# Performance work log

Hardware: AMD Instinct MI355X
Metric: run time of the kernel (lower is better)

Reference implementation:

```python
import jax, jax.numpy as jnp
import numpy as np

N = 50000   # nodes
DEG = 16    # avg degree
E = N * DEG # edges
D = 64      # 2*vl, vl=32
EPS = 1e-12 # F.normalize eps


def setup_inputs() -> dict:
    key = jax.random.key(0)
    k1, k2, k3, k4 = jax.random.split(key, 4)
    ft_lv0 = jax.random.normal(k1, (N, D), dtype=jnp.float32)
    # fc weights: Linear(4*vl, 2*vl, bias=False) -> shape [2*vl, 4*vl] = [64, 128]
    W1 = jax.random.normal(k2, (D, 2 * D), dtype=jnp.float32) * 0.05
    W2 = jax.random.normal(k3, (D, 2 * D), dtype=jnp.float32) * 0.05
    # edge list: tgt[e] gathers ft[nbr[e]] and sums into node tgt[e]
    nbr = jax.random.randint(k4, (E,), 0, N, dtype=jnp.int32)
    tgt = jnp.repeat(jnp.arange(N, dtype=jnp.int32), DEG)  # sorted segment ids
    return {"ft_lv0": ft_lv0, "W1": W1, "W2": W2, "nbr": nbr, "tgt": tgt}


def _gcn_layer(ft, W, nbr, tgt, n_nodes):
    # sum-pool neighbor features: pool[n] = sum_{m in adj(n)} ft[m]
    pool = jax.ops.segment_sum(ft[nbr], tgt, num_segments=n_nodes)  # [N, D]
    # concat(node + pool, node * pool); pool==0 for isolated nodes reproduces
    # the original else-branch cat(node, zeros) exactly.
    z = jnp.concatenate([ft + pool, ft * pool], axis=-1)  # [N, 2D]
    return jax.nn.relu(z @ W.T)  # [N, D]


def reference(ft_lv0, W1, W2, nbr, tgt):
    n_nodes = ft_lv0.shape[0]
    ft_lv1 = _gcn_layer(ft_lv0, W1, nbr, tgt, n_nodes)
    ft_lv2 = _gcn_layer(ft_lv1, W2, nbr, tgt, n_nodes)
    # F.normalize(z, dim=-1): z / max(||z||_2, eps)
    norm = jnp.linalg.norm(ft_lv2, axis=-1, keepdims=True)
    return ft_lv2 / jnp.maximum(norm, EPS)
```

## Files before the change

kernel.cpp:

```cpp
#include <hip/hip_runtime.h>
#include <hip/hip_bf16.h>


#define N_NODES 50000
#define DEG 16
#define DIM 64
#define NTILES 3125

typedef __attribute__((ext_vector_type(8))) short short8;
typedef __attribute__((ext_vector_type(8))) unsigned short ushort8;
typedef __attribute__((ext_vector_type(4))) float f32x4;

__device__ __forceinline__ unsigned short f2b(float f) {
  unsigned int u = __float_as_uint(f);
  u = (u + 0x7FFFu + ((u >> 16) & 1u)) >> 16;
  return (unsigned short)u;
}
#define LOF(u) __uint_as_float((u) << 16)
#define HIF(u) __uint_as_float((u) & 0xFFFF0000u)

__global__ void cast_bf16(const float* __restrict__ in, unsigned short* __restrict__ out, int n4) {
  const int i = blockIdx.x * 256 + threadIdx.x;
  if (i < n4) {
    const float4 v = reinterpret_cast<const float4*>(in)[i];
    ushort4 o4;
    o4.x = f2b(v.x); o4.y = f2b(v.y); o4.z = f2b(v.z); o4.w = f2b(v.w);
    reinterpret_cast<ushort4*>(out)[i] = o4;
  }
}

__global__ void prep_w(const float* __restrict__ W1, const float* __restrict__ W2,
                       unsigned short* __restrict__ Wb) {
  const int task = blockIdx.x * 256 + threadIdx.x;
  if (task >= 2048) return;
  const int which = task >> 10;
  const int f = (task >> 6) & 15;
  const int l = task & 63;
  const int ct = f >> 2, ks = f & 3;
  const int wn = l & 15, wg = l >> 4;
  const float* W = which ? W2 : W1;
  const float* wp = W + (ct * 16 + wn) * 128 + ks * 32 + wg * 8;
  const float4 w0 = *(const float4*)wp;
  const float4 w1 = *(const float4*)(wp + 4);
  ushort8 o;
  o[0] = f2b(w0.x); o[1] = f2b(w0.y); o[2] = f2b(w0.z); o[3] = f2b(w0.w);
  o[4] = f2b(w1.x); o[5] = f2b(w1.y); o[6] = f2b(w1.z); o[7] = f2b(w1.w);
  *(ushort8*)(Wb + ((size_t)(which * 16 + f) * 64 + l) * 8) = o;
}

#define GATHER_AND_STAGE()                                                     \
  _Pragma("unroll 2")                                                          \
  for (int p = 0; p < 8; ++p) {                                                \
    const int rA = (base + 2 * p) * DEG;                                       \
    const int4 ia0 = *(const int4*)(nbr + rA);                                 \
    const int4 ia1 = *(const int4*)(nbr + rA + 4);                             \
    const int4 ia2 = *(const int4*)(nbr + rA + 8);                             \
    const int4 ia3 = *(const int4*)(nbr + rA + 12);                            \
    const int4 ib0 = *(const int4*)(nbr + rA + 16);                            \
    const int4 ib1 = *(const int4*)(nbr + rA + 20);                            \
    const int4 ib2 = *(const int4*)(nbr + rA + 24);                            \
    const int4 ib3 = *(const int4*)(nbr + rA + 28);                            \
    const unsigned int un  = ftp[(base + 2 * p + half) * 32 + c];              \
    const unsigned int v0  = ftp[(half ? ib0.x : ia0.x) * 32 + c];             \
    const unsigned int v1  = ftp[(half ? ib0.y : ia0.y) * 32 + c];             \
    const unsigned int v2  = ftp[(half ? ib0.z : ia0.z) * 32 + c];             \
    const unsigned int v3  = ftp[(half ? ib0.w : ia0.w) * 32 + c];             \
    const unsigned int v4  = ftp[(half ? ib1.x : ia1.x) * 32 + c];             \
    const unsigned int v5  = ftp[(half ? ib1.y : ia1.y) * 32 + c];             \
    const unsigned int v6  = ftp[(half ? ib1.z : ia1.z) * 32 + c];             \
    const unsigned int v7  = ftp[(half ? ib1.w : ia1.w) * 32 + c];             \
    const unsigned int v8  = ftp[(half ? ib2.x : ia2.x) * 32 + c];             \
    const unsigned int v9  = ftp[(half ? ib2.y : ia2.y) * 32 + c];             \
    const unsigned int v10 = ftp[(half ? ib2.z : ia2.z) * 32 + c];             \
    const unsigned int v11 = ftp[(half ? ib2.w : ia2.w) * 32 + c];             \
    const unsigned int v12 = ftp[(half ? ib3.x : ia3.x) * 32 + c];             \
    const unsigned int v13 = ftp[(half ? ib3.y : ia3.y) * 32 + c];             \
    const unsigned int v14 = ftp[(half ? ib3.z : ia3.z) * 32 + c];             \
    const unsigned int v15 = ftp[(half ? ib3.w : ia3.w) * 32 + c];             \
    const float plo = (((LOF(v0) + LOF(v1)) + (LOF(v2) + LOF(v3))) +           \
                       ((LOF(v4) + LOF(v5)) + (LOF(v6) + LOF(v7)))) +          \
                      (((LOF(v8) + LOF(v9)) + (LOF(v10) + LOF(v11))) +         \
                       ((LOF(v12) + LOF(v13)) + (LOF(v14) + LOF(v15))));       \
    const float phi = (((HIF(v0) + HIF(v1)) + (HIF(v2) + HIF(v3))) +           \
                       ((HIF(v4) + HIF(v5)) + (HIF(v6) + HIF(v7)))) +          \
                      (((HIF(v8) + HIF(v9)) + (HIF(v10) + HIF(v11))) +         \
                       ((HIF(v12) + HIF(v13)) + (HIF(v14) + HIF(v15))));       \
    const float nlo = LOF(un), nhi = HIF(un);                                  \
    const float z1lo = nlo + plo, z1hi = nhi + phi;                            \
    const float z2lo = nlo * plo, z2hi = nhi * phi;                            \
    unsigned int z1p, z2p;                                                     \
    asm("v_cvt_pk_bf16_f32 %0, %1, %2" : "=v"(z1p) : "v"(z1lo), "v"(z1hi));    \
    asm("v_cvt_pk_bf16_f32 %0, %1, %2" : "=v"(z2p) : "v"(z2lo), "v"(z2hi));    \
    const int r = 2 * p + half;                                                \
    const int cs = c ^ ((r & 7) << 2);                                         \
    Az[wid][r * 64 + cs] = z1p;                                                \
    Az[wid][r * 64 + 32 + cs] = z2p;                                           \
  }

#define PRELOAD_W()                                                            \
  short8 Bf[4][4];                                                             \
  {                                                                            \
    const short8* wf = (const short8*)Wb;                                      \
    _Pragma("unroll")                                                          \
    for (int f = 0; f < 16; ++f) Bf[f >> 2][f & 3] = wf[f * 64 + lane];        \
  }

#define MFMA_ACCUM()                                                           \
  f32x4 ac0 = {0.f, 0.f, 0.f, 0.f}, ac1 = ac0, ac2 = ac0, ac3 = ac0;          \
  {                                                                            \
    const int arow = lane & 15, agrp = lane >> 4;                              \
    const int axor = (arow & 7) << 2;                                          \
    _Pragma("unroll")                                                          \
    for (int ks = 0; ks < 4; ++ks) {                                           \
      const short8 a =                                                         \
          *(const short8*)&Az[wid][arow * 64 + ((ks * 16 + agrp * 4) ^ axor)]; \
      ac0 = __builtin_amdgcn_mfma_f32_16x16x32_bf16(a, Bf[0][ks], ac0, 0, 0, 0);\
      ac1 = __builtin_amdgcn_mfma_f32_16x16x32_bf16(a, Bf[1][ks], ac1, 0, 0, 0);\
      ac2 = __builtin_amdgcn_mfma_f32_16x16x32_bf16(a, Bf[2][ks], ac2, 0, 0, 0);\
      ac3 = __builtin_amdgcn_mfma_f32_16x16x32_bf16(a, Bf[3][ks], ac3, 0, 0, 0);\
    }                                                                          \
  }

__global__ __launch_bounds__(256, 2)
void gcn_mfma1(const unsigned short* __restrict__ ftb,
               const unsigned short* __restrict__ Wb,
               const int* __restrict__ nbr,
               unsigned short* __restrict__ outb) {
  __shared__ unsigned int Az[4][1024];
  const int tid = threadIdx.x;
  const int lane = tid & 63, wid = tid >> 6;
  const int t = blockIdx.x * 4 + wid;
  if (t >= NTILES) return;
  const int base = t * 16;
  const int half = lane >> 5, c = lane & 31;
  const unsigned int* ftp = (const unsigned int*)ftb;

  GATHER_AND_STAGE();
  PRELOAD_W();
  MFMA_ACCUM();

  unsigned short* sh = (unsigned short*)&Az[wid][0];
  const int colf = lane & 15, rgrp = lane >> 4;
#define STAGE1(AC, CT)                                                         \
  _Pragma("unroll")                                                            \
  for (int rr = 0; rr < 4; ++rr)                                               \
    sh[(rgrp * 4 + rr) * 64 + (((CT)*16 + colf) ^ (rgrp << 4))] =              \
        f2b(fmaxf(AC[rr], 0.f));
  STAGE1(ac0, 0) STAGE1(ac1, 1) STAGE1(ac2, 2) STAGE1(ac3, 3)
#undef STAGE1
  const int row = lane >> 2, q = lane & 3;
  const int blk = q ^ (row >> 2);
  const ushort8 d0 = *(const ushort8*)&sh[row * 64 + q * 16];
  const ushort8 d1 = *(const ushort8*)&sh[row * 64 + q * 16 + 8];
  *(ushort8*)(outb + (base + row) * 64 + blk * 16) = d0;
  *(ushort8*)(outb + (base + row) * 64 + blk * 16 + 8) = d1;
}

__global__ __launch_bounds__(256, 2)
void gcn_mfma2(const unsigned short* __restrict__ ftb,
               const unsigned short* __restrict__ Wb,
               const int* __restrict__ nbr,
               float* __restrict__ out) {
  __shared__ unsigned int Az[4][1024];
  const int tid = threadIdx.x;
  const int lane = tid & 63, wid = tid >> 6;
  const int t = blockIdx.x * 4 + wid;
  if (t >= NTILES) return;
  const int base = t * 16;
  const int half = lane >> 5, c = lane & 31;
  const unsigned int* ftp = (const unsigned int*)ftb;

  GATHER_AND_STAGE();
  PRELOAD_W();
  MFMA_ACCUM();

  float v0[4], v1[4], v2[4], v3[4];
#pragma unroll
  for (int rr = 0; rr < 4; ++rr) {
    v0[rr] = fmaxf(ac0[rr], 0.f);
    v1[rr] = fmaxf(ac1[rr], 0.f);
    v2[rr] = fmaxf(ac2[rr], 0.f);
    v3[rr] = fmaxf(ac3[rr], 0.f);
  }
  float s0 = v0[0]*v0[0] + v1[0]*v1[0] + v2[0]*v2[0] + v3[0]*v3[0];
  float s1 = v0[1]*v0[1] + v1[1]*v1[1] + v2[1]*v2[1] + v3[1]*v3[1];
  float s2 = v0[2]*v0[2] + v1[2]*v1[2] + v2[2]*v2[2] + v3[2]*v3[2];
  float s3 = v0[3]*v0[3] + v1[3]*v1[3] + v2[3]*v2[3] + v3[3]*v3[3];
#pragma unroll
  for (int w = 1; w < 16; w <<= 1) {
    s0 += __shfl_xor(s0, w, 64);
    s1 += __shfl_xor(s1, w, 64);
    s2 += __shfl_xor(s2, w, 64);
    s3 += __shfl_xor(s3, w, 64);
  }
  const float kk[4] = {1.f / fmaxf(sqrtf(s0), 1e-12f),
                       1.f / fmaxf(sqrtf(s1), 1e-12f),
                       1.f / fmaxf(sqrtf(s2), 1e-12f),
                       1.f / fmaxf(sqrtf(s3), 1e-12f)};

  float* shf = (float*)&Az[wid][0];
  const int colf = lane & 15, rgrp = lane >> 4;
#define STAGE2(VA, CT)                                                         \
  _Pragma("unroll")                                                            \
  for (int rr = 0; rr < 4; ++rr)                                               \
    shf[(rgrp * 4 + rr) * 64 + (((CT)*16 + colf) ^ (rgrp << 4))] =             \
        VA[rr] * kk[rr];
  STAGE2(v0, 0) STAGE2(v1, 1) STAGE2(v2, 2) STAGE2(v3, 3)
#undef STAGE2
  const int row = lane >> 2, q = lane & 3;
  const int blk = q ^ (row >> 2);
  float* op = out + (size_t)(base + row) * 64 + blk * 16;
#pragma unroll
  for (int e = 0; e < 4; ++e)
    *(float4*)(op + e * 4) = *(const float4*)&shf[row * 64 + q * 16 + e * 4];
}

extern "C" void kernel_launch(void* const* d_in, const int* in_sizes, int n_in,
                              void* d_out, int out_size, void* d_ws, size_t ws_size,
                              hipStream_t stream) {
  const float* ft0;
  const float* W1;
  const float* W2;
  const int*   nbr;
  if (in_sizes[0] == N_NODES * DIM) {
    ft0 = (const float*)d_in[0];
    W1  = (const float*)d_in[1];
    W2  = (const float*)d_in[2];
    nbr = (const int*)d_in[3];
  } else {
    W1  = (const float*)d_in[0];
    W2  = (const float*)d_in[1];
    ft0 = (const float*)d_in[2];
    nbr = (const int*)d_in[3];
  }

  unsigned short* ftb0 = (unsigned short*)d_ws;
  unsigned short* ft1b = ftb0 + (size_t)N_NODES * DIM;
  unsigned short* Wb   = ft1b + (size_t)N_NODES * DIM;
  float* out = (float*)d_out;

  const int n4 = (N_NODES * DIM) / 4;
  cast_bf16<<<dim3((n4 + 255) / 256), dim3(256), 0, stream>>>(ft0, ftb0, n4);
  prep_w<<<dim3(8), dim3(256), 0, stream>>>(W1, W2, Wb);

  const int nblk = (NTILES + 3) / 4;
  gcn_mfma1<<<dim3(nblk), dim3(256), 0, stream>>>(ftb0, Wb, nbr, ft1b);
  gcn_mfma2<<<dim3(nblk), dim3(256), 0, stream>>>(ft1b, Wb + 8192, nbr, out);
}
```

Baseline: 116.4 us.

## Split each 16-row tile's gather across two waves sharing LDS

Each 16-node tile is now handled by two wavefronts. Each wave gathers and stages half of the rows into a shared LDS tile, the waves synchronise, and then both run the MFMA over the full tile. The epilogue store is split by row halves between the two waves. This doubles the waves working on the latency-bound neighbour gather per tile and raises launch_bounds occupancy to 4 blocks. In exchange it adds two __syncthreads per block and duplicates the MFMA and weight-register work in both waves.

New measurement: 114.2 us. Within noise of the previous version (-1.9%).

```diff
diff --git a/kernel.cpp b/kernel.cpp
--- a/kernel.cpp
+++ b/kernel.cpp
@@ -48,10 +48,11 @@
   *(ushort8*)(Wb + ((size_t)(which * 16 + f) * 64 + l) * 8) = o;
 }
 
-#define GATHER_AND_STAGE()                                                     \
+#define GATHER_AND_STAGE_V3()                                                  \
   _Pragma("unroll 2")                                                          \
-  for (int p = 0; p < 8; ++p) {                                                \
-    const int rA = (base + 2 * p) * DEG;                                       \
+  for (int p = 0; p < 4; ++p) {                                                \
+    const int pp = sub * 4 + p;                                                \
+    const int rA = (base + 2 * pp) * DEG;                                      \
     const int4 ia0 = *(const int4*)(nbr + rA);                                 \
     const int4 ia1 = *(const int4*)(nbr + rA + 4);                             \
     const int4 ia2 = *(const int4*)(nbr + rA + 8);                             \
@@ -60,7 +61,7 @@
     const int4 ib1 = *(const int4*)(nbr + rA + 20);                            \
     const int4 ib2 = *(const int4*)(nbr + rA + 24);                            \
     const int4 ib3 = *(const int4*)(nbr + rA + 28);                            \
-    const unsigned int un  = ftp[(base + 2 * p + half) * 32 + c];              \
+    const unsigned int un  = ftp[(base + 2 * pp + half) * 32 + c];             \
     const unsigned int v0  = ftp[(half ? ib0.x : ia0.x) * 32 + c];             \
     const unsigned int v1  = ftp[(half ? ib0.y : ia0.y) * 32 + c];             \
     const unsigned int v2  = ftp[(half ? ib0.z : ia0.z) * 32 + c];             \
@@ -91,10 +92,10 @@
     unsigned int z1p, z2p;                                                     \
     asm("v_cvt_pk_bf16_f32 %0, %1, %2" : "=v"(z1p) : "v"(z1lo), "v"(z1hi));    \
     asm("v_cvt_pk_bf16_f32 %0, %1, %2" : "=v"(z2p) : "v"(z2lo), "v"(z2hi));    \
-    const int r = 2 * p + half;                                                \
+    const int r = 2 * pp + half;                                               \
     const int cs = c ^ ((r & 7) << 2);                                         \
-    Az[wid][r * 64 + cs] = z1p;                                                \
-    Az[wid][r * 64 + 32 + cs] = z2p;                                           \
+    Azs[r * 64 + cs] = z1p;                                                    \
+    Azs[r * 64 + 32 + cs] = z2p;                                               \
   }
 
 #define PRELOAD_W()                                                            \
@@ -113,7 +114,7 @@
     _Pragma("unroll")                                                          \
     for (int ks = 0; ks < 4; ++ks) {                                           \
       const short8 a =                                                         \
-          *(const short8*)&Az[wid][arow * 64 + ((ks * 16 + agrp * 4) ^ axor)]; \
+          *(const short8*)&Azs[arow * 64 + ((ks * 16 + agrp * 4) ^ axor)];     \
       ac0 = __builtin_amdgcn_mfma_f32_16x16x32_bf16(a, Bf[0][ks], ac0, 0, 0, 0);\
       ac1 = __builtin_amdgcn_mfma_f32_16x16x32_bf16(a, Bf[1][ks], ac1, 0, 0, 0);\
       ac2 = __builtin_amdgcn_mfma_f32_16x16x32_bf16(a, Bf[2][ks], ac2, 0, 0, 0);\
@@ -121,98 +122,115 @@
     }                                                                          \
   }
 
-__global__ __launch_bounds__(256, 2)
+__global__ __launch_bounds__(256, 4)
 void gcn_mfma1(const unsigned short* __restrict__ ftb,
                const unsigned short* __restrict__ Wb,
                const int* __restrict__ nbr,
                unsigned short* __restrict__ outb) {
-  __shared__ unsigned int Az[4][1024];
+  __shared__ unsigned int Az[2][1024];
   const int tid = threadIdx.x;
   const int lane = tid & 63, wid = tid >> 6;
-  const int t = blockIdx.x * 4 + wid;
-  if (t >= NTILES) return;
+  const int tl = wid >> 1, sub = wid & 1;
+  const int t = __builtin_amdgcn_readfirstlane(blockIdx.x * 2 + tl);
+  const bool active = (t < NTILES);
   const int base = t * 16;
   const int half = lane >> 5, c = lane & 31;
   const unsigned int* ftp = (const unsigned int*)ftb;
-
-  GATHER_AND_STAGE();
+  unsigned int* Azs = &Az[tl][0];
+
+  if (active) { GATHER_AND_STAGE_V3(); }
   PRELOAD_W();
+  __syncthreads();
   MFMA_ACCUM();
-
-  unsigned short* sh = (unsigned short*)&Az[wid][0];
-  const int colf = lane & 15, rgrp = lane >> 4;
-#define STAGE1(AC, CT)                                                         \
-  _Pragma("unroll")                                                            \
-  for (int rr = 0; rr < 4; ++rr)                                               \
-    sh[(rgrp * 4 + rr) * 64 + (((CT)*16 + colf) ^ (rgrp << 4))] =              \
-        f2b(fmaxf(AC[rr], 0.f));
-  STAGE1(ac0, 0) STAGE1(ac1, 1) STAGE1(ac2, 2) STAGE1(ac3, 3)
-#undef STAGE1
-  const int row = lane >> 2, q = lane & 3;
-  const int blk = q ^ (row >> 2);
-  const ushort8 d0 = *(const ushort8*)&sh[row * 64 + q * 16];
-  const ushort8 d1 = *(const ushort8*)&sh[row * 64 + q * 16 + 8];
-  *(ushort8*)(outb + (base + row) * 64 + blk * 16) = d0;
-  *(ushort8*)(outb + (base + row) * 64 + blk * 16 + 8) = d1;
-}
-
-__global__ __launch_bounds__(256, 2)
+  __syncthreads();
+
+  if (active) {
+    unsigned short* sh = (unsigned short*)Azs;
+    const int colf = lane & 15, rgrp = lane >> 4;
+    if ((rgrp >> 1) == sub) {
+#define STG1(AC, CT)                                                           \
+      _Pragma("unroll")                                                        \
+      for (int rr = 0; rr < 4; ++rr)                                           \
+        sh[(rgrp * 4 + rr) * 64 + (((CT)*16 + colf) ^ (rgrp << 4))] =          \
+            f2b(fmaxf(AC[rr], 0.f));
+      STG1(ac0, 0) STG1(ac1, 1) STG1(ac2, 2) STG1(ac3, 3)
+#undef STG1
+    }
+    const int row = sub * 8 + (lane >> 3), b = lane & 7;
+    const int rg = row >> 2;
+    const ushort8 d = *(const ushort8*)&sh[row * 64 + ((b ^ (rg << 1)) << 3)];
+    *(ushort8*)(outb + (size_t)(base + row) * 64 + b * 8) = d;
+  }
+}
+
+__global__ __launch_bounds__(256, 4)
 void gcn_mfma2(const unsigned short* __restrict__ ftb,
                const unsigned short* __restrict__ Wb,
                const int* __restrict__ nbr,
                float* __restrict__ out) {
-  __shared__ unsigned int Az[4][1024];
+  __shared__ unsigned int Az[2][1024];
   const int tid = threadIdx.x;
   const int lane = tid & 63, wid = tid >> 6;
-  const int t = blockIdx.x * 4 + wid;
-  if (t >= NTILES) return;
+  const int tl = wid >> 1, sub = wid & 1;
+  const int t = __builtin_amdgcn_readfirstlane(blockIdx.x * 2 + tl);
+  const bool active = (t < NTILES);
   const int base = t * 16;
   const int half = lane >> 5, c = lane & 31;
   const unsigned int* ftp = (const unsigned int*)ftb;
-
-  GATHER_AND_STAGE();
+  unsigned int* Azs = &Az[tl][0];
+
+  if (active) { GATHER_AND_STAGE_V3(); }
   PRELOAD_W();
+  __syncthreads();
   MFMA_ACCUM();
-
-  float v0[4], v1[4], v2[4], v3[4];
+  __syncthreads();
+
+  if (active) {
+    float v0[4], v1[4], v2[4], v3[4];
 #pragma unroll
-  for (int rr = 0; rr < 4; ++rr) {
-    v0[rr] = fmaxf(ac0[rr], 0.f);
-    v1[rr] = fmaxf(ac1[rr], 0.f);
-    v2[rr] = fmaxf(ac2[rr], 0.f);
-    v3[rr] = fmaxf(ac3[rr], 0.f);
-  }
-  float s0 = v0[0]*v0[0] + v1[0]*v1[0] + v2[0]*v2[0] + v3[0]*v3[0];
-  float s1 = v0[1]*v0[1] + v1[1]*v1[1] + v2[1]*v2[1] + v3[1]*v3[1];
-  float s2 = v0[2]*v0[2] + v1[2]*v1[2] + v2[2]*v2[2] + v3[2]*v3[2];
-  float s3 = v0[3]*v0[3] + v1[3]*v1[3] + v2[3]*v2[3] + v3[3]*v3[3];
+    for (int rr = 0; rr < 4; ++rr) {
+      v0[rr] = fmaxf(ac0[rr], 0.f);
+      v1[rr] = fmaxf(ac1[rr], 0.f);
+      v2[rr] = fmaxf(ac2[rr], 0.f);
+      v3[rr] = fmaxf(ac3[rr], 0.f);
+    }
+    float s0 = v0[0]*v0[0] + v1[0]*v1[0] + v2[0]*v2[0] + v3[0]*v3[0];
+    float s1 = v0[1]*v0[1] + v1[1]*v1[1] + v2[1]*v2[1] + v3[1]*v3[1];
+    float s2 = v0[2]*v0[2] + v1[2]*v1[2] + v2[2]*v2[2] + v3[2]*v3[2];
+    float s3 = v0[3]*v0[3] + v1[3]*v1[3] + v2[3]*v2[3] + v3[3]*v3[3];
 #pragma unroll
-  for (int w = 1; w < 16; w <<= 1) {
-    s0 += __shfl_xor(s0, w, 64);
-    s1 += __shfl_xor(s1, w, 64);
-    s2 += __shfl_xor(s2, w, 64);
-    s3 += __shfl_xor(s3, w, 64);
-  }
-  const float kk[4] = {1.f / fmaxf(sqrtf(s0), 1e-12f),
-                       1.f / fmaxf(sqrtf(s1), 1e-12f),
-                       1.f / fmaxf(sqrtf(s2), 1e-12f),
-                       1.f / fmaxf(sqrtf(s3), 1e-12f)};
-
-  float* shf = (float*)&Az[wid][0];
-  const int colf = lane & 15, rgrp = lane >> 4;
-#define STAGE2(VA, CT)                                                         \
-  _Pragma("unroll")                                                            \
-  for (int rr = 0; rr < 4; ++rr)                                               \
-    shf[(rgrp * 4 + rr) * 64 + (((CT)*16 + colf) ^ (rgrp << 4))] =             \
-        VA[rr] * kk[rr];
-  STAGE2(v0, 0) STAGE2(v1, 1) STAGE2(v2, 2) STAGE2(v3, 3)
-#undef STAGE2
-  const int row = lane >> 2, q = lane & 3;
-  const int blk = q ^ (row >> 2);
-  float* op = out + (size_t)(base + row) * 64 + blk * 16;
+    for (int w = 1; w < 16; w <<= 1) {
+      s0 += __shfl_xor(s0, w, 64);
+      s1 += __shfl_xor(s1, w, 64);
+      s2 += __shfl_xor(s2, w, 64);
+      s3 += __shfl_xor(s3, w, 64);
+    }
+    const float kk[4] = {1.f / fmaxf(sqrtf(s0), 1e-12f),
+                         1.f / fmaxf(sqrtf(s1), 1e-12f),
+                         1.f / fmaxf(sqrtf(s2), 1e-12f),
+                         1.f / fmaxf(sqrtf(s3), 1e-12f)};
+
+    float* shf = (float*)Azs;
+    const int colf = lane & 15, rgrp = lane >> 4;
+    if ((rgrp >> 1) == sub) {
+#define STG2(VA, CT)                                                           \
+      _Pragma("unroll")                                                        \
+      for (int rr = 0; rr < 4; ++rr)                                           \
+        shf[(rgrp * 4 + rr) * 64 + (((CT)*16 + colf) ^ (rgrp << 4))] =         \
+            VA[rr] * kk[rr];
+      STG2(v0, 0) STG2(v1, 1) STG2(v2, 2) STG2(v3, 3)
+#undef STG2
+    }
+    const int row = sub * 8 + (lane >> 3);
+    const int rg = row >> 2;
+    float* op = out + (size_t)(base + row) * 64;
 #pragma unroll
-  for (int e = 0; e < 4; ++e)
-    *(float4*)(op + e * 4) = *(const float4*)&shf[row * 64 + q * 16 + e * 4];
+    for (int e = 0; e < 2; ++e) {
+      const int c4 = (lane & 7) * 2 + e;
+      *(float4*)(op + c4 * 4) =
+          *(const float4*)&shf[row * 64 + ((c4 ^ (rg << 2)) << 2)];
+    }
+  }
 }
 
 extern "C" void kernel_launch(void* const* d_in, const int* in_sizes, int n_in,
@@ -243,7 +261,7 @@
   cast_bf16<<<dim3((n4 + 255) / 256), dim3(256), 0, stream>>>(ft0, ftb0, n4);
   prep_w<<<dim3(8), dim3(256), 0, stream>>>(W1, W2, Wb);
 
-  const int nblk = (NTILES + 3) / 4;
+  const int nblk = (NTILES + 1) / 2;
   gcn_mfma1<<<dim3(nblk), dim3(256), 0, stream>>>(ftb0, Wb, nbr, ft1b);
   gcn_mfma2<<<dim3(nblk), dim3(256), 0, stream>>>(ft1b, Wb + 8192, nbr, out);
 }
```
